# Kernel optimization log

Hardware: AMD Instinct MI355X
Metric: run time of the kernel (lower is better)

## Reference

```python
import jax, jax.numpy as jnp
import numpy as np

B, T, NM = 128, 2048, 8  # batch, nSteps, nMaxwell


def setup_inputs() -> dict:
    key = jax.random.key(0)
    k1, k2, k3 = jax.random.split(key, 3)
    S_e = jax.random.normal(k1, (B, T, 3, 3), dtype=jnp.float32)
    # strictly increasing times per batch element
    dt = jax.random.uniform(k2, (B, T), minval=0.01, maxval=0.1, dtype=jnp.float32)
    t = jnp.cumsum(dt, axis=1)
    # [tau_1..tau_nM, g_infy, g_1..g_nM] -> last dim 2*NM + 1
    PronyParams = jax.random.uniform(k3, (B, T, 2 * NM + 1), minval=0.1, maxval=1.0, dtype=jnp.float32)
    return {"S_e": S_e, "t": t, "PronyParams": PronyParams}


def reference(S_e, t, PronyParams):
    """Viscoelastic 2nd Piola-Kirchhoff stress via recursive Prony update.

    S_e:         [B, T, 3, 3] instantaneous elastic stress
    t:           [B, T] time
    PronyParams: [B, T, 2*nM+1] (relaxation times tau then coefficients g)
    Returns (S, S_infy, Q_sum), each [B, T, 3, 3].
    """
    nM = PronyParams.shape[-1] // 2
    tau = PronyParams[..., :nM]                      # [B,T,nM]
    g = PronyParams[..., nM:]                        # [B,T,nM+1]
    g = g / jnp.sum(g, axis=-1, keepdims=True)
    g_infy = g[..., 0:1]                             # [B,T,1]
    g_i = g[..., 1:]                                 # [B,T,nM]

    Bsz = S_e.shape[0]
    # time-major scan inputs
    xs = (
        jnp.swapaxes(t, 0, 1),      # [T,B]
        jnp.swapaxes(S_e, 0, 1),    # [T,B,3,3]
        jnp.swapaxes(tau, 0, 1),    # [T,B,nM]
        jnp.swapaxes(g_i, 0, 1),    # [T,B,nM]
    )
    init = (
        jnp.zeros((Bsz, nM, 3, 3), S_e.dtype),  # Q_0
        -t[:, 1],                                # t_prev (as in original initializer)
        jnp.zeros((Bsz, 3, 3), S_e.dtype),       # S_prev
        tau[:, 0],
        g_i[:, 0],
    )

    def step(carry, x):
        Q_p, t_p, S_p, tau_p, g_p = carry
        t_c, S_c, tau_c, g_c = x
        g_bar = 0.5 * (g_c + g_p)                 # [B,nM]
        tau_bar = 0.5 * (tau_c + tau_p)           # [B,nM]
        dt = (t_c - t_p)[:, None]                 # [B,1]
        e = jnp.exp(-0.5 * dt / tau_bar)          # exp(-dt/(2 tau_bar))
        term1 = (e * e)[..., None, None]          # exp(-dt/tau_bar), [B,nM,1,1]
        term2 = (e * g_bar)[..., None, None]      # [B,nM,1,1]
        dS = (S_c - S_p)[:, None]                 # [B,1,3,3]
        Q = term1 * Q_p + term2 * dS              # [B,nM,3,3]
        return (Q, t_c, S_c, tau_c, g_c), Q

    _, Qs = jax.lax.scan(step, init, xs)          # [T,B,nM,3,3]
    Q_sum = jnp.swapaxes(jnp.sum(Qs, axis=2), 0, 1)  # [B,T,3,3]
    S_infy = g_infy[..., None] * S_e              # [B,T,1,1] * [B,T,3,3]
    S = S_infy + Q_sum
    return (S, S_infy, Q_sum)
```

## Files before the change

kernel.cpp:

```cpp
#include <hip/hip_runtime.h>

#define T_LEN 2048
#define NMODE 8
#define NPP   17

template <int L, bool PHASE3>
__global__ __launch_bounds__(256)
void scan_fused(const float* __restrict__ Se,
                const float* __restrict__ tt,
                const float* __restrict__ pp,
                float* __restrict__ R,
                float* __restrict__ P,
                float* __restrict__ out,
                int B) {
    constexpr int NC = T_LEN / L;
    int tid = blockIdx.x * blockDim.x + threadIdx.x;
    int total = B * NC * 9;
    if (tid >= total) return;
    int e  = tid % 9;
    int bc = tid / 9;
    int c  = bc % NC;
    int b  = bc / NC;
    int t0 = c * L;

    float tau_p[NMODE], g_p[NMODE];
    float inv_p, t_p, S_p;
    {
        int prow = (t0 == 0) ? 0 : (t0 - 1);
        size_t row = (size_t)b * T_LEN + prow;
        const float* p = pp + row * NPP;
        float gsum = 0.f;
        #pragma unroll
        for (int m = 0; m < NMODE; ++m) tau_p[m] = p[m];
        float g8 = p[8];
        #pragma unroll
        for (int m = 0; m < NMODE; ++m) g_p[m] = p[9 + m];
        gsum = g8;
        #pragma unroll
        for (int m = 0; m < NMODE; ++m) gsum += g_p[m];
        inv_p = __builtin_amdgcn_rcpf(gsum);
        t_p = (t0 == 0) ? -tt[(size_t)b * T_LEN + 1] : tt[row];
        S_p = (t0 == 0) ? 0.f : Se[row * 9 + (size_t)e];
    }

    size_t rbase = ((size_t)(b * 9 + e) * NC + (size_t)c) * NMODE;

    float Q[NMODE], Pp[NMODE];
    if (PHASE3) {
        const float4* rz = (const float4*)(R + rbase);
        float4 z0 = rz[0], z1 = rz[1];
        Q[0]=z0.x; Q[1]=z0.y; Q[2]=z0.z; Q[3]=z0.w;
        Q[4]=z1.x; Q[5]=z1.y; Q[6]=z1.z; Q[7]=z1.w;
    } else {
        #pragma unroll
        for (int m = 0; m < NMODE; ++m) { Q[m] = 0.f; Pp[m] = 1.0f; }
    }

    const size_t nOut = (size_t)B * T_LEN * 9;

    #pragma unroll 2
    for (int s = 0; s < L; ++s) {
        size_t row = (size_t)b * T_LEN + (t0 + s);
        const float* p = pp + row * NPP;

        float tau_c[NMODE], g_c[NMODE];
        #pragma unroll
        for (int m = 0; m < NMODE; ++m) tau_c[m] = p[m];
        float g8 = p[8];
        #pragma unroll
        for (int m = 0; m < NMODE; ++m) g_c[m] = p[9 + m];
        float t_c = tt[row];
        float S_c = Se[row * 9 + (size_t)e];

        float gsum = g8;
        #pragma unroll
        for (int m = 0; m < NMODE; ++m) gsum += g_c[m];
        float inv_c = __builtin_amdgcn_rcpf(gsum);

        float mhdt = -0.5f * (t_c - t_p);
        float dS   = S_c - S_p;
        float qsum = 0.f;

        #pragma unroll
        for (int m = 0; m < NMODE; ++m) {
            float tau_b = 0.5f * (tau_c[m] + tau_p[m]);
            float g_b   = 0.5f * (g_c[m] * inv_c + g_p[m] * inv_p);
            float ee    = __expf(mhdt * __builtin_amdgcn_rcpf(tau_b));
            float A     = ee * ee;
            Q[m] = A * Q[m] + (ee * g_b) * dS;
            if (!PHASE3) Pp[m] *= A;
            else         qsum  += Q[m];
            tau_p[m] = tau_c[m];
            g_p[m]   = g_c[m];
        }
        inv_p = inv_c;
        t_p   = t_c;
        S_p   = S_c;

        if (PHASE3) {
            size_t sidx = row * 9 + (size_t)e;
            float sinf = (g8 * inv_c) * S_c;
            out[sidx]            = sinf + qsum;
            out[nOut + sidx]     = sinf;
            out[2 * nOut + sidx] = qsum;
        }
    }

    if (!PHASE3) {
        float4* rz = (float4*)(R + rbase);
        rz[0] = make_float4(Q[0], Q[1], Q[2], Q[3]);
        rz[1] = make_float4(Q[4], Q[5], Q[6], Q[7]);
        if (e == 0) {
            float4* pz = (float4*)(P + ((size_t)b * NC + (size_t)c) * NMODE);
            pz[0] = make_float4(Pp[0], Pp[1], Pp[2], Pp[3]);
            pz[1] = make_float4(Pp[4], Pp[5], Pp[6], Pp[7]);
        }
    }
}

template <int K>
__global__ __launch_bounds__(256)
void chunk_scan_wave(float* __restrict__ R, const float* __restrict__ P,
                     int B) {
    constexpr int NC = K * 64;
    int gtid = blockIdx.x * blockDim.x + threadIdx.x;
    int wid  = gtid >> 6;
    int lane = gtid & 63;
    if (wid >= B * 9) return;
    int e = wid % 9;
    int b = wid / 9;

    float* rp       = R + ((size_t)(b * 9 + e) * NC) * NMODE;
    const float* pq = P + ((size_t)b * NC) * NMODE;

    float pk[K][NMODE], rk[K][NMODE];
    float pa[NMODE], ra[NMODE];
    #pragma unroll
    for (int m = 0; m < NMODE; ++m) { pa[m] = 1.f; ra[m] = 0.f; }

    #pragma unroll
    for (int k = 0; k < K; ++k) {
        int c = lane * K + k;
        const float4* rv = (const float4*)(rp + (size_t)c * NMODE);
        const float4* pv = (const float4*)(pq + (size_t)c * NMODE);
        float4 r0 = rv[0], r1 = rv[1], p0 = pv[0], p1 = pv[1];
        rk[k][0]=r0.x; rk[k][1]=r0.y; rk[k][2]=r0.z; rk[k][3]=r0.w;
        rk[k][4]=r1.x; rk[k][5]=r1.y; rk[k][6]=r1.z; rk[k][7]=r1.w;
        pk[k][0]=p0.x; pk[k][1]=p0.y; pk[k][2]=p0.z; pk[k][3]=p0.w;
        pk[k][4]=p1.x; pk[k][5]=p1.y; pk[k][6]=p1.z; pk[k][7]=p1.w;
        #pragma unroll
        for (int m = 0; m < NMODE; ++m) {
            ra[m] = pk[k][m] * ra[m] + rk[k][m];
            pa[m] = pk[k][m] * pa[m];
        }
    }

    #pragma unroll
    for (int d = 1; d < 64; d <<= 1) {
        #pragma unroll
        for (int m = 0; m < NMODE; ++m) {
            float plo = __shfl_up(pa[m], d);
            float rlo = __shfl_up(ra[m], d);
            if (lane >= d) {
                ra[m] = pa[m] * rlo + ra[m];
                pa[m] = pa[m] * plo;
            }
        }
    }

    float z[NMODE];
    #pragma unroll
    for (int m = 0; m < NMODE; ++m) {
        float zz = __shfl_up(ra[m], 1);
        z[m] = (lane == 0) ? 0.f : zz;
    }

    #pragma unroll
    for (int k = 0; k < K; ++k) {
        int c = lane * K + k;
        float4* rv = (float4*)(rp + (size_t)c * NMODE);
        rv[0] = make_float4(z[0], z[1], z[2], z[3]);
        rv[1] = make_float4(z[4], z[5], z[6], z[7]);
        #pragma unroll
        for (int m = 0; m < NMODE; ++m)
            z[m] = pk[k][m] * z[m] + rk[k][m];
    }
}

template <int L>
static void run_pipeline(const float* Se, const float* tt, const float* pp,
                         float* out, float* ws, int B, hipStream_t stream) {
    constexpr int NC = T_LEN / L;
    constexpr int K  = NC / 64;
    float* R = ws;
    float* P = R + (size_t)B * 9 * NC * NMODE;

    dim3 blk(256);
    int tot1  = B * NC * 9;
    int grid1 = (tot1 + 255) / 256;
    int tot2  = B * 9 * 64;
    int grid2 = (tot2 + 255) / 256;

    scan_fused<L, false><<<grid1, blk, 0, stream>>>(Se, tt, pp, R, P, nullptr, B);
    chunk_scan_wave<K><<<grid2, blk, 0, stream>>>(R, P, B);
    scan_fused<L, true><<<grid1, blk, 0, stream>>>(Se, tt, pp, R, P, out, B);
}

extern "C" void kernel_launch(void* const* d_in, const int* in_sizes, int n_in,
                              void* d_out, int out_size, void* d_ws, size_t ws_size,
                              hipStream_t stream) {
    const float* Se = (const float*)d_in[0];
    const float* tt = (const float*)d_in[1];
    const float* pp = (const float*)d_in[2];
    float* out = (float*)d_out;
    float* ws  = (float*)d_ws;

    int B = in_sizes[1] / T_LEN;

    auto need = [&](int NC) {
        return ((size_t)B * 9 * NC * NMODE + (size_t)B * NC * NMODE) * sizeof(float);
    };

    if (need(T_LEN / 8) <= ws_size) {
        run_pipeline<8>(Se, tt, pp, out, ws, B, stream);
    } else if (need(T_LEN / 16) <= ws_size) {
        run_pipeline<16>(Se, tt, pp, out, ws, B, stream);
    } else {
        run_pipeline<32>(Se, tt, pp, out, ws, B, stream);
    }
}
```

Measured before the change: 120.6 us.

## Process three stress components per thread to share exp work across elements

Each thread in the chunk-scan kernels now handles three of the nine stress components instead of one, so the Prony parameter loads, reciprocals and exponentials are computed once and reused for three components. Blocks shrink to 128 threads, a smaller chunk length L=4 is tried first when the workspace allows, and the tau averaging is folded into the reciprocal. This cuts redundant transcendental work and parameter traffic. The cost is more registers per thread and fewer threads. The shorter chunks also make the middle chunk-scan pass larger.

```diff
diff --git a/kernel.cpp b/kernel.cpp
--- a/kernel.cpp
+++ b/kernel.cpp
@@ -5,55 +5,65 @@
 #define NPP   17
 
 template <int L, bool PHASE3>
-__global__ __launch_bounds__(256)
-void scan_fused(const float* __restrict__ Se,
-                const float* __restrict__ tt,
-                const float* __restrict__ pp,
-                float* __restrict__ R,
-                float* __restrict__ P,
-                float* __restrict__ out,
-                int B) {
+__global__ __launch_bounds__(128)
+void scan_fused3(const float* __restrict__ Se,
+                 const float* __restrict__ tt,
+                 const float* __restrict__ pp,
+                 float* __restrict__ R,
+                 float* __restrict__ P,
+                 float* __restrict__ out,
+                 int B) {
     constexpr int NC = T_LEN / L;
     int tid = blockIdx.x * blockDim.x + threadIdx.x;
-    int total = B * NC * 9;
+    int total = B * NC * 3;
     if (tid >= total) return;
-    int e  = tid % 9;
-    int bc = tid / 9;
+    int eg = tid % 3;
+    int bc = tid / 3;
     int c  = bc % NC;
     int b  = bc / NC;
     int t0 = c * L;
+    int e0 = eg * 3;
 
     float tau_p[NMODE], g_p[NMODE];
-    float inv_p, t_p, S_p;
+    float inv_p, t_p, S_p[3];
     {
         int prow = (t0 == 0) ? 0 : (t0 - 1);
         size_t row = (size_t)b * T_LEN + prow;
         const float* p = pp + row * NPP;
-        float gsum = 0.f;
         #pragma unroll
         for (int m = 0; m < NMODE; ++m) tau_p[m] = p[m];
         float g8 = p[8];
         #pragma unroll
         for (int m = 0; m < NMODE; ++m) g_p[m] = p[9 + m];
-        gsum = g8;
+        float gsum = g8;
         #pragma unroll
         for (int m = 0; m < NMODE; ++m) gsum += g_p[m];
         inv_p = __builtin_amdgcn_rcpf(gsum);
         t_p = (t0 == 0) ? -tt[(size_t)b * T_LEN + 1] : tt[row];
-        S_p = (t0 == 0) ? 0.f : Se[row * 9 + (size_t)e];
-    }
-
-    size_t rbase = ((size_t)(b * 9 + e) * NC + (size_t)c) * NMODE;
-
-    float Q[NMODE], Pp[NMODE];
+        if (t0 == 0) {
+            S_p[0] = S_p[1] = S_p[2] = 0.f;
+        } else {
+            const float* sp = Se + row * 9 + e0;
+            S_p[0] = sp[0]; S_p[1] = sp[1]; S_p[2] = sp[2];
+        }
+    }
+
+    float Q[NMODE][3], Pp[NMODE];
     if (PHASE3) {
-        const float4* rz = (const float4*)(R + rbase);
-        float4 z0 = rz[0], z1 = rz[1];
-        Q[0]=z0.x; Q[1]=z0.y; Q[2]=z0.z; Q[3]=z0.w;
-        Q[4]=z1.x; Q[5]=z1.y; Q[6]=z1.z; Q[7]=z1.w;
+        #pragma unroll
+        for (int j = 0; j < 3; ++j) {
+            size_t rb = ((size_t)(b * 9 + e0 + j) * NC + (size_t)c) * NMODE;
+            const float4* rz = (const float4*)(R + rb);
+            float4 z0 = rz[0], z1 = rz[1];
+            Q[0][j]=z0.x; Q[1][j]=z0.y; Q[2][j]=z0.z; Q[3][j]=z0.w;
+            Q[4][j]=z1.x; Q[5][j]=z1.y; Q[6][j]=z1.z; Q[7][j]=z1.w;
+        }
     } else {
         #pragma unroll
-        for (int m = 0; m < NMODE; ++m) { Q[m] = 0.f; Pp[m] = 1.0f; }
+        for (int m = 0; m < NMODE; ++m) {
+            Q[m][0] = Q[m][1] = Q[m][2] = 0.f;
+            Pp[m] = 1.0f;
+        }
     }
 
     const size_t nOut = (size_t)B * T_LEN * 9;
@@ -70,47 +80,61 @@
         #pragma unroll
         for (int m = 0; m < NMODE; ++m) g_c[m] = p[9 + m];
         float t_c = tt[row];
-        float S_c = Se[row * 9 + (size_t)e];
+        const float* sc = Se + row * 9 + e0;
+        float S_c[3] = { sc[0], sc[1], sc[2] };
 
         float gsum = g8;
         #pragma unroll
         for (int m = 0; m < NMODE; ++m) gsum += g_c[m];
         float inv_c = __builtin_amdgcn_rcpf(gsum);
 
-        float mhdt = -0.5f * (t_c - t_p);
-        float dS   = S_c - S_p;
-        float qsum = 0.f;
-
-        #pragma unroll
-        for (int m = 0; m < NMODE; ++m) {
-            float tau_b = 0.5f * (tau_c[m] + tau_p[m]);
-            float g_b   = 0.5f * (g_c[m] * inv_c + g_p[m] * inv_p);
-            float ee    = __expf(mhdt * __builtin_amdgcn_rcpf(tau_b));
-            float A     = ee * ee;
-            Q[m] = A * Q[m] + (ee * g_b) * dS;
+        float ndt = t_p - t_c;
+        float dS[3] = { S_c[0]-S_p[0], S_c[1]-S_p[1], S_c[2]-S_p[2] };
+        float qs0 = 0.f, qs1 = 0.f, qs2 = 0.f;
+
+        #pragma unroll
+        for (int m = 0; m < NMODE; ++m) {
+            float ee  = __expf(ndt * __builtin_amdgcn_rcpf(tau_c[m] + tau_p[m]));
+            float A   = ee * ee;
+            float g_b = 0.5f * (g_c[m] * inv_c + g_p[m] * inv_p);
+            float eC  = ee * g_b;
+            Q[m][0] = A * Q[m][0] + eC * dS[0];
+            Q[m][1] = A * Q[m][1] + eC * dS[1];
+            Q[m][2] = A * Q[m][2] + eC * dS[2];
             if (!PHASE3) Pp[m] *= A;
-            else         qsum  += Q[m];
+            else { qs0 += Q[m][0]; qs1 += Q[m][1]; qs2 += Q[m][2]; }
             tau_p[m] = tau_c[m];
             g_p[m]   = g_c[m];
         }
         inv_p = inv_c;
         t_p   = t_c;
-        S_p   = S_c;
+        S_p[0] = S_c[0]; S_p[1] = S_c[1]; S_p[2] = S_c[2];
 
         if (PHASE3) {
-            size_t sidx = row * 9 + (size_t)e;
-            float sinf = (g8 * inv_c) * S_c;
-            out[sidx]            = sinf + qsum;
-            out[nOut + sidx]     = sinf;
-            out[2 * nOut + sidx] = qsum;
+            size_t sidx = row * 9 + (size_t)e0;
+            float gi = g8 * inv_c;
+            float sf0 = gi * S_c[0], sf1 = gi * S_c[1], sf2 = gi * S_c[2];
+            out[sidx]     = sf0 + qs0;
+            out[sidx + 1] = sf1 + qs1;
+            out[sidx + 2] = sf2 + qs2;
+            out[nOut + sidx]     = sf0;
+            out[nOut + sidx + 1] = sf1;
+            out[nOut + sidx + 2] = sf2;
+            out[2*nOut + sidx]     = qs0;
+            out[2*nOut + sidx + 1] = qs1;
+            out[2*nOut + sidx + 2] = qs2;
         }
     }
 
     if (!PHASE3) {
-        float4* rz = (float4*)(R + rbase);
-        rz[0] = make_float4(Q[0], Q[1], Q[2], Q[3]);
-        rz[1] = make_float4(Q[4], Q[5], Q[6], Q[7]);
-        if (e == 0) {
+        #pragma unroll
+        for (int j = 0; j < 3; ++j) {
+            size_t rb = ((size_t)(b * 9 + e0 + j) * NC + (size_t)c) * NMODE;
+            float4* rz = (float4*)(R + rb);
+            rz[0] = make_float4(Q[0][j], Q[1][j], Q[2][j], Q[3][j]);
+            rz[1] = make_float4(Q[4][j], Q[5][j], Q[6][j], Q[7][j]);
+        }
+        if (eg == 0) {
             float4* pz = (float4*)(P + ((size_t)b * NC + (size_t)c) * NMODE);
             pz[0] = make_float4(Pp[0], Pp[1], Pp[2], Pp[3]);
             pz[1] = make_float4(Pp[4], Pp[5], Pp[6], Pp[7]);
@@ -195,15 +219,14 @@
     float* R = ws;
     float* P = R + (size_t)B * 9 * NC * NMODE;
 
-    dim3 blk(256);
-    int tot1  = B * NC * 9;
-    int grid1 = (tot1 + 255) / 256;
+    int tot1  = B * NC * 3;
+    int grid1 = (tot1 + 127) / 128;
     int tot2  = B * 9 * 64;
     int grid2 = (tot2 + 255) / 256;
 
-    scan_fused<L, false><<<grid1, blk, 0, stream>>>(Se, tt, pp, R, P, nullptr, B);
-    chunk_scan_wave<K><<<grid2, blk, 0, stream>>>(R, P, B);
-    scan_fused<L, true><<<grid1, blk, 0, stream>>>(Se, tt, pp, R, P, out, B);
+    scan_fused3<L, false><<<grid1, dim3(128), 0, stream>>>(Se, tt, pp, R, P, nullptr, B);
+    chunk_scan_wave<K><<<grid2, dim3(256), 0, stream>>>(R, P, B);
+    scan_fused3<L, true><<<grid1, dim3(128), 0, stream>>>(Se, tt, pp, R, P, out, B);
 }
 
 extern "C" void kernel_launch(void* const* d_in, const int* in_sizes, int n_in,
@@ -221,7 +244,9 @@
         return ((size_t)B * 9 * NC * NMODE + (size_t)B * NC * NMODE) * sizeof(float);
     };
 
-    if (need(T_LEN / 8) <= ws_size) {
+    if (need(T_LEN / 4) <= ws_size) {
+        run_pipeline<4>(Se, tt, pp, out, ws, B, stream);
+    } else if (need(T_LEN / 8) <= ws_size) {
         run_pipeline<8>(Se, tt, pp, out, ws, B, stream);
     } else if (need(T_LEN / 16) <= ws_size) {
         run_pipeline<16>(Se, tt, pp, out, ws, B, stream);
```

New measurement: 132.4 us. +9.8%, slower.

## Restructure chunked scan into per-block mode-parallel pass with linear correction phase

Applied to the files above, without the earlier changes.

Phase A now runs one block per (batch, chunk), stages inputs in shared memory, and assigns one thread per (element, mode). It computes the local Q sums and cumulative decay products in a single pass and writes partial outputs plus the per-step decay factors. Phase C then adds the carry-in contribution as a linear correction (sum over modes of cumulative decay times the chunk-start state) instead of re-running the scan. This removes the second recurrence pass and its redundant parameter loads, at the cost of extra workspace traffic for the decay factors and an output read-modify-write. The workspace size check is dropped and L is fixed at 16.

```diff
diff --git a/kernel.cpp b/kernel.cpp
--- a/kernel.cpp
+++ b/kernel.cpp
@@ -4,118 +4,97 @@
 #define NMODE 8
 #define NPP   17
 
-template <int L, bool PHASE3>
-__global__ __launch_bounds__(256)
-void scan_fused(const float* __restrict__ Se,
-                const float* __restrict__ tt,
-                const float* __restrict__ pp,
-                float* __restrict__ R,
-                float* __restrict__ P,
-                float* __restrict__ out,
-                int B) {
+template <int L>
+__global__ __launch_bounds__(128)
+void phaseA(const float* __restrict__ Se,
+            const float* __restrict__ tt,
+            const float* __restrict__ pp,
+            float* __restrict__ out,
+            float* __restrict__ partR,
+            float* __restrict__ partP,
+            float* __restrict__ caA,
+            int B) {
     constexpr int NC = T_LEN / L;
-    int tid = blockIdx.x * blockDim.x + threadIdx.x;
-    int total = B * NC * 9;
-    if (tid >= total) return;
-    int e  = tid % 9;
-    int bc = tid / 9;
-    int c  = bc % NC;
-    int b  = bc / NC;
-    int t0 = c * L;
-
-    float tau_p[NMODE], g_p[NMODE];
-    float inv_p, t_p, S_p;
+    const int tid = threadIdx.x;
+    const int c   = blockIdx.x % NC;
+    const int b   = blockIdx.x / NC;
+    const int t0  = c * L;
+    const int r0  = (c == 0) ? 0 : t0 - 1;
+    const int off = (c == 0) ? 0 : 1;
+
+    __shared__ float s_pp[(L + 1) * NPP];
+    __shared__ float s_Se[(L + 1) * 9];
+    __shared__ float s_t[L + 1];
+    __shared__ float s_inv[L + 1];
+    __shared__ float s_sf[L * 9];
+    __shared__ float s_q[L * 9];
+    __shared__ float s_ca[L * 8];
+
     {
-        int prow = (t0 == 0) ? 0 : (t0 - 1);
-        size_t row = (size_t)b * T_LEN + prow;
-        const float* p = pp + row * NPP;
-        float gsum = 0.f;
-        #pragma unroll
-        for (int m = 0; m < NMODE; ++m) tau_p[m] = p[m];
-        float g8 = p[8];
-        #pragma unroll
-        for (int m = 0; m < NMODE; ++m) g_p[m] = p[9 + m];
-        gsum = g8;
-        #pragma unroll
-        for (int m = 0; m < NMODE; ++m) gsum += g_p[m];
-        inv_p = __builtin_amdgcn_rcpf(gsum);
-        t_p = (t0 == 0) ? -tt[(size_t)b * T_LEN + 1] : tt[row];
-        S_p = (t0 == 0) ? 0.f : Se[row * 9 + (size_t)e];
-    }
-
-    size_t rbase = ((size_t)(b * 9 + e) * NC + (size_t)c) * NMODE;
-
-    float Q[NMODE], Pp[NMODE];
-    if (PHASE3) {
-        const float4* rz = (const float4*)(R + rbase);
-        float4 z0 = rz[0], z1 = rz[1];
-        Q[0]=z0.x; Q[1]=z0.y; Q[2]=z0.z; Q[3]=z0.w;
-        Q[4]=z1.x; Q[5]=z1.y; Q[6]=z1.z; Q[7]=z1.w;
-    } else {
-        #pragma unroll
-        for (int m = 0; m < NMODE; ++m) { Q[m] = 0.f; Pp[m] = 1.0f; }
-    }
+        const float* src = pp + ((size_t)b * T_LEN + r0) * NPP;
+        for (int i = tid; i < (L + 1) * NPP; i += 128) s_pp[i] = src[i];
+        const float* ss = Se + ((size_t)b * T_LEN + r0) * 9;
+        for (int i = tid; i < (L + 1) * 9; i += 128) s_Se[i] = ss[i];
+        const float* st = tt + ((size_t)b * T_LEN + r0);
+        if (tid < L + 1) s_t[tid] = st[tid];
+    }
+    __syncthreads();
+    if (tid < L + 1) {
+        float g = 0.f;
+        #pragma unroll
+        for (int k = 8; k < NPP; ++k) g += s_pp[tid * NPP + k];
+        s_inv[tid] = __builtin_amdgcn_rcpf(g);
+    }
+    __syncthreads();
+
+    const bool act = tid < 72;
+    const int  e   = tid >> 3;
+    const int  m   = tid & 7;
+
+    float tau_p = s_pp[m];
+    float gq_p  = s_pp[9 + m] * s_inv[0];
+    float t_p   = (c == 0) ? -tt[(size_t)b * T_LEN + 1] : s_t[0];
+    float S_p   = (c == 0) ? 0.f : (act ? s_Se[e] : 0.f);
+
+    float Q = 0.f, cA = 1.f;
+    #pragma unroll
+    for (int s = 0; s < L; ++s) {
+        const int rc = s + off;
+        float tau_c = s_pp[rc * NPP + m];
+        float inv_c = s_inv[rc];
+        float gq_c  = s_pp[rc * NPP + 9 + m] * inv_c;
+        float t_c   = s_t[rc];
+        float S_c   = act ? s_Se[rc * 9 + e] : 0.f;
+        float ee = __expf((t_p - t_c) * __builtin_amdgcn_rcpf(tau_c + tau_p));
+        float A  = ee * ee;
+        float eC = ee * 0.5f * (gq_c + gq_p);
+        Q   = A * Q + eC * (S_c - S_p);
+        cA *= A;
+        float qs = Q;
+        qs += __shfl_xor(qs, 1);
+        qs += __shfl_xor(qs, 2);
+        qs += __shfl_xor(qs, 4);
+        if (act && m == 0) {
+            s_sf[s * 9 + e] = s_pp[rc * NPP + 8] * inv_c * S_c;
+            s_q[s * 9 + e]  = qs;
+        }
+        if (tid < 8) s_ca[s * 8 + m] = cA;
+        tau_p = tau_c; gq_p = gq_c; t_p = t_c; S_p = S_c;
+    }
+
+    if (act) partR[((size_t)(b * 9 + e) * NC + c) * 8 + m] = Q;
+    if (tid < 8) partP[((size_t)b * NC + c) * 8 + m] = cA;
+
+    __syncthreads();
 
     const size_t nOut = (size_t)B * T_LEN * 9;
-
-    #pragma unroll 2
-    for (int s = 0; s < L; ++s) {
-        size_t row = (size_t)b * T_LEN + (t0 + s);
-        const float* p = pp + row * NPP;
-
-        float tau_c[NMODE], g_c[NMODE];
-        #pragma unroll
-        for (int m = 0; m < NMODE; ++m) tau_c[m] = p[m];
-        float g8 = p[8];
-        #pragma unroll
-        for (int m = 0; m < NMODE; ++m) g_c[m] = p[9 + m];
-        float t_c = tt[row];
-        float S_c = Se[row * 9 + (size_t)e];
-
-        float gsum = g8;
-        #pragma unroll
-        for (int m = 0; m < NMODE; ++m) gsum += g_c[m];
-        float inv_c = __builtin_amdgcn_rcpf(gsum);
-
-        float mhdt = -0.5f * (t_c - t_p);
-        float dS   = S_c - S_p;
-        float qsum = 0.f;
-
-        #pragma unroll
-        for (int m = 0; m < NMODE; ++m) {
-            float tau_b = 0.5f * (tau_c[m] + tau_p[m]);
-            float g_b   = 0.5f * (g_c[m] * inv_c + g_p[m] * inv_p);
-            float ee    = __expf(mhdt * __builtin_amdgcn_rcpf(tau_b));
-            float A     = ee * ee;
-            Q[m] = A * Q[m] + (ee * g_b) * dS;
-            if (!PHASE3) Pp[m] *= A;
-            else         qsum  += Q[m];
-            tau_p[m] = tau_c[m];
-            g_p[m]   = g_c[m];
-        }
-        inv_p = inv_c;
-        t_p   = t_c;
-        S_p   = S_c;
-
-        if (PHASE3) {
-            size_t sidx = row * 9 + (size_t)e;
-            float sinf = (g8 * inv_c) * S_c;
-            out[sidx]            = sinf + qsum;
-            out[nOut + sidx]     = sinf;
-            out[2 * nOut + sidx] = qsum;
-        }
-    }
-
-    if (!PHASE3) {
-        float4* rz = (float4*)(R + rbase);
-        rz[0] = make_float4(Q[0], Q[1], Q[2], Q[3]);
-        rz[1] = make_float4(Q[4], Q[5], Q[6], Q[7]);
-        if (e == 0) {
-            float4* pz = (float4*)(P + ((size_t)b * NC + (size_t)c) * NMODE);
-            pz[0] = make_float4(Pp[0], Pp[1], Pp[2], Pp[3]);
-            pz[1] = make_float4(Pp[4], Pp[5], Pp[6], Pp[7]);
-        }
-    }
+    float* o = out + ((size_t)b * T_LEN + t0) * 9;
+    for (int i = tid; i < L * 9; i += 128) {
+        o[nOut + i]     = s_sf[i];
+        o[2 * nOut + i] = s_q[i];
+    }
+    float* ca = caA + ((size_t)b * NC + c) * (L * 8);
+    for (int i = tid; i < L * 8; i += 128) ca[i] = s_ca[i];
 }
 
 template <int K>
@@ -188,22 +167,46 @@
 }
 
 template <int L>
-static void run_pipeline(const float* Se, const float* tt, const float* pp,
-                         float* out, float* ws, int B, hipStream_t stream) {
+__global__ __launch_bounds__(128)
+void phaseC(float* __restrict__ out,
+            const float* __restrict__ partR,
+            const float* __restrict__ caA,
+            int B) {
     constexpr int NC = T_LEN / L;
-    constexpr int K  = NC / 64;
-    float* R = ws;
-    float* P = R + (size_t)B * 9 * NC * NMODE;
-
-    dim3 blk(256);
-    int tot1  = B * NC * 9;
-    int grid1 = (tot1 + 255) / 256;
-    int tot2  = B * 9 * 64;
-    int grid2 = (tot2 + 255) / 256;
-
-    scan_fused<L, false><<<grid1, blk, 0, stream>>>(Se, tt, pp, R, P, nullptr, B);
-    chunk_scan_wave<K><<<grid2, blk, 0, stream>>>(R, P, B);
-    scan_fused<L, true><<<grid1, blk, 0, stream>>>(Se, tt, pp, R, P, out, B);
+    const int tid = threadIdx.x;
+    const int c   = blockIdx.x % NC;
+    const int b   = blockIdx.x / NC;
+
+    __shared__ float s_Z[72];
+    __shared__ float s_ca[L * 8];
+    __shared__ float s_q[L * 9];
+    __shared__ float s_sf[L * 9];
+
+    if (tid < 72) {
+        int e = tid >> 3, m = tid & 7;
+        s_Z[tid] = partR[((size_t)(b * 9 + e) * NC + c) * 8 + m];
+    }
+    const float* ca = caA + ((size_t)b * NC + c) * (L * 8);
+    for (int i = tid; i < L * 8; i += 128) s_ca[i] = ca[i];
+
+    const size_t nOut = (size_t)B * T_LEN * 9;
+    float* o = out + ((size_t)b * T_LEN + (size_t)c * L) * 9;
+    for (int i = tid; i < L * 9; i += 128) {
+        s_sf[i] = o[nOut + i];
+        s_q[i]  = o[2 * nOut + i];
+    }
+    __syncthreads();
+
+    for (int i = tid; i < L * 9; i += 128) {
+        int t = i / 9, e = i - t * 9;
+        float corr = 0.f;
+        #pragma unroll
+        for (int m = 0; m < NMODE; ++m)
+            corr += s_ca[t * 8 + m] * s_Z[e * 8 + m];
+        float qs = s_q[i] + corr;
+        o[i]            = s_sf[i] + qs;
+        o[2 * nOut + i] = qs;
+    }
 }
 
 extern "C" void kernel_launch(void* const* d_in, const int* in_sizes, int n_in,
@@ -213,19 +216,22 @@
     const float* tt = (const float*)d_in[1];
     const float* pp = (const float*)d_in[2];
     float* out = (float*)d_out;
-    float* ws  = (float*)d_ws;
 
     int B = in_sizes[1] / T_LEN;
 
-    auto need = [&](int NC) {
-        return ((size_t)B * 9 * NC * NMODE + (size_t)B * NC * NMODE) * sizeof(float);
-    };
-
-    if (need(T_LEN / 8) <= ws_size) {
-        run_pipeline<8>(Se, tt, pp, out, ws, B, stream);
-    } else if (need(T_LEN / 16) <= ws_size) {
-        run_pipeline<16>(Se, tt, pp, out, ws, B, stream);
-    } else {
-        run_pipeline<32>(Se, tt, pp, out, ws, B, stream);
-    }
-}
+    constexpr int L  = 16;
+    constexpr int NC = T_LEN / L;
+    constexpr int K  = NC / 64;
+
+    float* partR = (float*)d_ws;
+    float* partP = partR + (size_t)B * 9 * NC * 8;
+    float* caA   = partP + (size_t)B * NC * 8;
+
+    int gridA = B * NC;
+    int gridB = (B * 9 * 64 + 255) / 256;
+
+    phaseA<L><<<gridA, dim3(128), 0, stream>>>(Se, tt, pp, out,
+                                               partR, partP, caA, B);
+    chunk_scan_wave<K><<<gridB, dim3(256), 0, stream>>>(partR, partP, B);
+    phaseC<L><<<gridA, dim3(128), 0, stream>>>(out, partR, caA, B);
+}
```

New measurement: 135.0 us. 11.9% more time.
